# Kernel tuning notes

Hardware: AMD Instinct MI355X
Metric: run time of the kernel (lower is better)

The kernel has to match this reference:

```python
import jax, jax.numpy as jnp
import numpy as np

HID = 128
NLAYERS = 8
LAT = 32
DIM_IN = 63 + 15 + LAT  # pe(xyz,L=10)=3+60, pe(shift,L=2)=3+12, latent=32 -> 110


def _pe(x, L):
    # NeRF positional encoding, include_input=True, freq-major [sin3,cos3] per freq
    freqs = (2.0 ** jnp.arange(L)).astype(x.dtype)
    xf = x[..., None, :] * freqs[:, None]                      # [..., L, 3]
    sc = jnp.concatenate([jnp.sin(xf), jnp.cos(xf)], axis=-1)  # [..., L, 6]
    return jnp.concatenate([x, sc.reshape(*x.shape[:-1], 6 * L)], axis=-1)


def setup_inputs() -> dict:
    key = jax.random.key(0)
    ks = jax.random.split(key, 24)
    B, P, V = 2, 32768, 5023
    d = {}
    d["pts"] = jax.random.normal(ks[0], (B, P, 3), jnp.float32)
    d["deformed_mesh_pts"] = jax.random.normal(ks[1], (B, V, 3), jnp.float32)
    d["cano_verts"] = jax.random.normal(ks[2], (1, V, 3), jnp.float32)
    d["motion_latent"] = jax.random.normal(ks[3], (B, P, LAT), jnp.float32)
    for i in range(NLAYERS):
        fin = DIM_IN if i == 0 else (DIM_IN + HID if i == NLAYERS // 2 else HID)
        d[f"w{i}"] = jax.random.normal(ks[4 + i], (HID, fin), jnp.float32) / np.sqrt(fin).astype(np.float32)
        d[f"b{i}"] = jnp.zeros((HID,), jnp.float32)
    d["w_out"] = jax.random.normal(ks[20], (3, HID), jnp.float32) * 0.01
    d["b_out"] = jnp.zeros((3,), jnp.float32)
    return d


def reference(pts, deformed_mesh_pts, cano_verts, motion_latent,
              w0, b0, w1, b1, w2, b2, w3, b3, w4, b4, w5, b5, w6, b6, w7, b7,
              w_out, b_out):
    # mesh-guided shift per vertex
    mesh_shift = cano_verts - deformed_mesh_pts                 # [B,V,3]
    # point-to-point NN search (squared euclidean cdist + argmin)
    d2 = ((pts ** 2).sum(-1)[:, :, None]
          + (deformed_mesh_pts ** 2).sum(-1)[:, None, :]
          - 2.0 * jnp.einsum('bpc,bvc->bpv', pts, deformed_mesh_pts))  # [B,P,V]
    d2 = jnp.maximum(d2, 0.0)
    idx = jnp.argmin(d2, axis=-1)                               # [B,P]
    dist = jnp.min(d2, axis=-1)                                 # [B,P]
    weight = jnp.exp(-dist)[..., None]                          # 1/exp(dist)
    gidx = jnp.broadcast_to(idx[:, :, None], idx.shape + (3,))
    gshift = jnp.take_along_axis(mesh_shift, gidx, axis=1) * weight  # [B,P,3]
    # deformation MLP with skip connection at layer 4
    initial = jnp.concatenate([_pe(pts, 10), _pe(gshift, 2), motion_latent], axis=-1)
    ws = [w0, w1, w2, w3, w4, w5, w6, w7]
    bs = [b0, b1, b2, b3, b4, b5, b6, b7]
    x = initial
    last_feat = x
    for i in range(NLAYERS):
        inp = jnp.concatenate([initial, x], axis=-1) if i == NLAYERS // 2 else x
        x = inp @ ws[i].T + bs[i]
        last_feat = x  # pre-activation feature (out_feat_ls[-1])
        x = jax.nn.relu(x)
    mlp_shift = x @ w_out.T + b_out                             # [B,P,3]
    pts_shifts = gshift + mlp_shift
    return pts + pts_shifts, last_feat
```

## Files before the change

### kernel.cpp

```cpp
#include <hip/hip_runtime.h>
#include <math.h>

typedef unsigned short ushort_t;
typedef unsigned int   uint_t;
typedef __attribute__((ext_vector_type(8)))  short bf16x8;
typedef __attribute__((ext_vector_type(16))) float f32x16;
typedef __attribute__((ext_vector_type(2)))  float f32x2;

#define NPTS   65536
#define NV     5023
#define NVP    5120
#define NPRB   2560
#define LATD   32
#define KF     110
#define FSTR   112
#define MARGIN 2.0e-3f

__device__ __forceinline__ ushort_t f2bf(float f) {
  union { float f; unsigned u; } x; x.f = f;
  unsigned r = x.u + 0x7fffu + ((x.u >> 16) & 1u);
  return (ushort_t)(r >> 16);
}
__device__ __forceinline__ float bf2f(ushort_t u) {
  union { unsigned u; float f; } x; x.u = ((unsigned)u) << 16;
  return x.f;
}
__device__ __forceinline__ uint_t packsplit(float v) {
  const ushort_t h = f2bf(v);
  const ushort_t l = f2bf(v - bf2f(h));
  return (uint_t)h | ((uint_t)l << 16);
}

__device__ __forceinline__ void dbl_step(float& s, float& c) {
  const float t = s * c;
  const float cn = fmaf(-2.f * s, s, 1.f);
  s = t + t;
  c = cn;
}

__global__ __launch_bounds__(256) void k_prep(
    const float* __restrict__ dm,
    const float* __restrict__ w0, const float* __restrict__ w1,
    const float* __restrict__ w2, const float* __restrict__ w3,
    const float* __restrict__ w4, const float* __restrict__ w5,
    const float* __restrict__ w6, const float* __restrict__ w7,
    ushort_t* __restrict__ wsWh, ushort_t* __restrict__ wsWl,
    float4* __restrict__ vpreA, float4* __restrict__ vpreB)
{
  const int e = blockIdx.x * 256 + threadIdx.x;
  {
    const int p = e >> 14, local = e & 16383;
    const int j   = local & 7;
    const int lh  = (local >> 3) & 1;
    const int l31 = (local >> 4) & 31;
    const int tn  = (local >> 9) & 3;
    const int ks  = (local >> 11) & 7;
    const int n = tn*32 + l31;
    const int k = ks*16 + lh*8 + j;
    float v;
    if (p == 0)      v = (k < KF) ? w0[n*110 + k] : 0.f;
    else if (p == 1) v = w1[n*128 + k];
    else if (p == 2) v = w2[n*128 + k];
    else if (p == 3) v = w3[n*128 + k];
    else if (p == 4) v = (k < KF) ? w4[n*238 + k] : 0.f;
    else if (p == 5) v = w4[n*238 + KF + k];
    else if (p == 6) v = w5[n*128 + k];
    else if (p == 7) v = w6[n*128 + k];
    else             v = w7[n*128 + k];
    const ushort_t h = f2bf(v);
    wsWh[e] = h;
    wsWl[e] = f2bf(v - bf2f(h));
  }
  if (e < 2*NPRB) {
    const int b  = (e >= NPRB) ? 1 : 0;
    const int pr = e - b*NPRB;
    const float* __restrict__ dmb = dm + b*NV*3;
    const int v0 = 2*pr, v1 = v0 + 1;
    float x0=0.f, y0=0.f, z0=0.f, w0v=3.0e38f;
    float x1=0.f, y1=0.f, z1=0.f, w1v=3.0e38f;
    if (v0 < NV) {
      x0 = dmb[v0*3+0]; y0 = dmb[v0*3+1]; z0 = dmb[v0*3+2];
      w0v = fmaf(x0,x0, fmaf(y0,y0, z0*z0));
    }
    if (v1 < NV) {
      x1 = dmb[v1*3+0]; y1 = dmb[v1*3+1]; z1 = dmb[v1*3+2];
      w1v = fmaf(x1,x1, fmaf(y1,y1, z1*z1));
    }
    vpreA[b*NPRB + pr] = make_float4(x0, x1, y0, y1);
    vpreB[b*NPRB + pr] = make_float4(z0, z1, w0v, w1v);
  }
}

__global__ __launch_bounds__(256, 4) void k_nnfeat(
    const float* __restrict__ pts, const float* __restrict__ dm,
    const float* __restrict__ cano, const float* __restrict__ lat,
    const float4* __restrict__ vpreA, const float4* __restrict__ vpreB,
    uint_t* __restrict__ feat, float* __restrict__ base3)
{
  __shared__ __align__(16) float4 sVa[256];
  __shared__ __align__(16) float4 sVb[256];
  __shared__ float sD[64];
  __shared__ int   sI[64];

  const int tid = threadIdx.x;
  const int lane = tid & 63, w = tid >> 6;
  const int slot = lane >> 4, s = lane & 15;
  const int g0 = blockIdx.x * 64;
  const int b  = blockIdx.x >> 9;
  const int pbase = g0 + w*16 + slot*4;

  const float4* __restrict__ vA = vpreA + b*NPRB;
  const float4* __restrict__ vB = vpreB + b*NPRB;

  f32x2 MX[4], MY[4], MZ[4];
  float p2[4];
  #pragma unroll
  for (int j = 0; j < 4; ++j) {
    const float px = pts[(pbase+j)*3+0], py = pts[(pbase+j)*3+1], pz = pts[(pbase+j)*3+2];
    p2[j] = fmaf(px,px, fmaf(py,py, pz*pz));
    MX[j] = (f32x2){-2.f*px, -2.f*px};
    MY[j] = (f32x2){-2.f*py, -2.f*py};
    MZ[j] = (f32x2){-2.f*pz, -2.f*pz};
  }

  float gm[5][4];
  #pragma unroll
  for (int sc = 0; sc < 5; ++sc) {
    f32x2 m0 = {3.0e38f, 3.0e38f}, m1 = m0, m2 = m0, m3 = m0;
    #pragma unroll
    for (int h = 0; h < 2; ++h) {
      const int c = sc*2 + h;
      __syncthreads();
      sVa[tid] = vA[c*256 + tid];
      sVb[tid] = vB[c*256 + tid];
      __syncthreads();
      #pragma unroll 8
      for (int kk = 0; kk < 16; ++kk) {
        const int pr = kk*16 + s;
        const float4 qa = sVa[pr];
        const float4 qb = sVb[pr];
        const f32x2 xx = {qa.x, qa.y}, yy = {qa.z, qa.w};
        const f32x2 zz = {qb.x, qb.y}, ww = {qb.z, qb.w};
        f32x2 t;
        t = __builtin_elementwise_fma(xx, MX[0], ww);
        t = __builtin_elementwise_fma(yy, MY[0], t);
        t = __builtin_elementwise_fma(zz, MZ[0], t);
        m0 = __builtin_elementwise_min(m0, t);
        t = __builtin_elementwise_fma(xx, MX[1], ww);
        t = __builtin_elementwise_fma(yy, MY[1], t);
        t = __builtin_elementwise_fma(zz, MZ[1], t);
        m1 = __builtin_elementwise_min(m1, t);
        t = __builtin_elementwise_fma(xx, MX[2], ww);
        t = __builtin_elementwise_fma(yy, MY[2], t);
        t = __builtin_elementwise_fma(zz, MZ[2], t);
        m2 = __builtin_elementwise_min(m2, t);
        t = __builtin_elementwise_fma(xx, MX[3], ww);
        t = __builtin_elementwise_fma(yy, MY[3], t);
        t = __builtin_elementwise_fma(zz, MZ[3], t);
        m3 = __builtin_elementwise_min(m3, t);
      }
    }
    gm[sc][0] = fminf(m0.x, m0.y);
    gm[sc][1] = fminf(m1.x, m1.y);
    gm[sc][2] = fminf(m2.x, m2.y);
    gm[sc][3] = fminf(m3.x, m3.y);
  }

  float thr[4];
  #pragma unroll
  for (int j = 0; j < 4; ++j) {
    float mv = gm[0][j];
    #pragma unroll
    for (int sc = 1; sc < 5; ++sc) mv = fminf(mv, gm[sc][j]);
    #pragma unroll
    for (int off = 1; off <= 8; off <<= 1)
      mv = fminf(mv, __shfl_xor(mv, off, 64));
    thr[j] = mv + MARGIN;
  }

  float bs[4]; int bi[4];
  #pragma unroll
  for (int j = 0; j < 4; ++j) { bs[j] = 3.4e38f; bi[j] = 0; }
  uint_t hm = 0;
  #pragma unroll
  for (int sc = 0; sc < 5; ++sc)
    if (gm[sc][0] <= thr[0] || gm[sc][1] <= thr[1] ||
        gm[sc][2] <= thr[2] || gm[sc][3] <= thr[3]) hm |= (1u << sc);
  while (hm) {
    const int sc = __ffs(hm) - 1; hm &= hm - 1;
    const int prb = sc*512;
    #pragma unroll 4
    for (int kk = 0; kk < 32; ++kk) {
      const int pr = prb + kk*16 + s;
      const float4 qa = vA[pr];
      const float4 qb = vB[pr];
      const int vi0 = 2*pr;
      #pragma unroll
      for (int j = 0; j < 4; ++j) {
        const float px = -0.5f*MX[j].x, py = -0.5f*MY[j].x, pz = -0.5f*MZ[j].x;
        {
          const float dot = fmaf(px, qa.x, fmaf(py, qa.z, pz*qb.x));
          float d2 = fmaf(-2.f, dot, p2[j] + qb.z);
          d2 = fmaxf(d2, 0.f);
          if (d2 < bs[j]) { bs[j] = d2; bi[j] = vi0; }
        }
        {
          const float dot = fmaf(px, qa.y, fmaf(py, qa.w, pz*qb.y));
          float d2 = fmaf(-2.f, dot, p2[j] + qb.w);
          d2 = fmaxf(d2, 0.f);
          if (d2 < bs[j]) { bs[j] = d2; bi[j] = vi0 + 1; }
        }
      }
    }
  }

  #pragma unroll
  for (int off = 1; off <= 8; off <<= 1) {
    #pragma unroll
    for (int j = 0; j < 4; ++j) {
      const float ob = __shfl_xor(bs[j], off, 64);
      const int   oi = __shfl_xor(bi[j], off, 64);
      const bool take = (ob < bs[j]) || ((ob == bs[j]) && (oi < bi[j]));
      if (take) { bs[j] = ob; bi[j] = oi; }
    }
  }
  if (s == 0) {
    #pragma unroll
    for (int j = 0; j < 4; ++j) {
      sD[w*16 + slot*4 + j] = bs[j];
      sI[w*16 + slot*4 + j] = bi[j];
    }
  }
  __syncthreads();

  const int p = tid & 63, slice = tid >> 6;
  const int g = g0 + p;
  const float wd = sD[p];
  const int   wi = sI[p];
  const float* __restrict__ dmb = dm + b * NV * 3;

  const float qx = pts[g*3+0], qy = pts[g*3+1], qz = pts[g*3+2];
  const float wgt = expf(-wd);
  const float sx = (cano[wi*3+0] - dmb[wi*3+0]) * wgt;
  const float sy = (cano[wi*3+1] - dmb[wi*3+1]) * wgt;
  const float sz = (cano[wi*3+2] - dmb[wi*3+2]) * wgt;

  uint_t* __restrict__ fr = feat + (size_t)g * FSTR;

  if (slice == 0) {
    base3[g*3+0] = qx + sx; base3[g*3+1] = qy + sy; base3[g*3+2] = qz + sz;
    fr[0] = packsplit(qx); fr[1] = packsplit(qy); fr[2] = packsplit(qz);
    float s0,c0,s1,c1,s2,c2;
    sincosf(qx,&s0,&c0); sincosf(qy,&s1,&c1); sincosf(qz,&s2,&c2);
    #pragma unroll
    for (int f = 0; f < 3; ++f) {
      const int k = 3 + 6*f;
      fr[k+0]=packsplit(s0); fr[k+1]=packsplit(s1); fr[k+2]=packsplit(s2);
      fr[k+3]=packsplit(c0); fr[k+4]=packsplit(c1); fr[k+5]=packsplit(c2);
      if (f < 2) { dbl_step(s0,c0); dbl_step(s1,c1); dbl_step(s2,c2); }
    }
    fr[110] = 0; fr[111] = 0;
  } else if (slice == 1) {
    float s0,c0,s1,c1,s2,c2;
    sincosf(qx*8.f,&s0,&c0); sincosf(qy*8.f,&s1,&c1); sincosf(qz*8.f,&s2,&c2);
    #pragma unroll
    for (int f = 3; f < 7; ++f) {
      const int k = 3 + 6*f;
      fr[k+0]=packsplit(s0); fr[k+1]=packsplit(s1); fr[k+2]=packsplit(s2);
      fr[k+3]=packsplit(c0); fr[k+4]=packsplit(c1); fr[k+5]=packsplit(c2);
      if (f < 6) { dbl_step(s0,c0); dbl_step(s1,c1); dbl_step(s2,c2); }
    }
  } else if (slice == 2) {
    float s0,c0,s1,c1,s2,c2;
    sincosf(qx*128.f,&s0,&c0); sincosf(qy*128.f,&s1,&c1); sincosf(qz*128.f,&s2,&c2);
    #pragma unroll
    for (int f = 7; f < 10; ++f) {
      const int k = 3 + 6*f;
      fr[k+0]=packsplit(s0); fr[k+1]=packsplit(s1); fr[k+2]=packsplit(s2);
      fr[k+3]=packsplit(c0); fr[k+4]=packsplit(c1); fr[k+5]=packsplit(c2);
      if (f < 9) { dbl_step(s0,c0); dbl_step(s1,c1); dbl_step(s2,c2); }
    }
    #pragma unroll
    for (int j = 0; j < 16; ++j) fr[78+j] = packsplit(lat[g*LATD + j]);
  } else {
    fr[63]=packsplit(sx); fr[64]=packsplit(sy); fr[65]=packsplit(sz);
    float s0,c0,s1,c1,s2,c2;
    sincosf(sx,&s0,&c0); sincosf(sy,&s1,&c1); sincosf(sz,&s2,&c2);
    #pragma unroll
    for (int f = 0; f < 2; ++f) {
      const int k = 66 + 6*f;
      fr[k+0]=packsplit(s0); fr[k+1]=packsplit(s1); fr[k+2]=packsplit(s2);
      fr[k+3]=packsplit(c0); fr[k+4]=packsplit(c1); fr[k+5]=packsplit(c2);
      if (f < 1) { dbl_step(s0,c0); dbl_step(s1,c1); dbl_step(s2,c2); }
    }
    #pragma unroll
    for (int j = 16; j < 32; ++j) fr[78+j] = packsplit(lat[g*LATD + j]);
  }
}


union U4 { uint_t u[4]; bf16x8 v; };

__device__ __forceinline__ void zero4(f32x16 (&a)[4]) {
  #pragma unroll
  for (int i = 0; i < 4; ++i) a[i] = (f32x16)(0.f);
}

__device__ __forceinline__ void load_feat_frags(
    const uint_t* __restrict__ fr, bf16x8 (&Xh)[8], bf16x8 (&Xl)[8], int lh)
{
  #pragma unroll
  for (int ks = 0; ks < 7; ++ks) {
    const int k0 = ks*16 + lh*8;
    const uint4 ua = *(const uint4*)(fr + k0);
    const uint4 ub = *(const uint4*)(fr + k0 + 4);
    U4 H, L;
    H.u[0] = (ua.x & 0xffffu) | (ua.y << 16);
    H.u[1] = (ua.z & 0xffffu) | (ua.w << 16);
    H.u[2] = (ub.x & 0xffffu) | (ub.y << 16);
    H.u[3] = (ub.z & 0xffffu) | (ub.w << 16);
    L.u[0] = (ua.x >> 16) | (ua.y & 0xffff0000u);
    L.u[1] = (ua.z >> 16) | (ua.w & 0xffff0000u);
    L.u[2] = (ub.x >> 16) | (ub.y & 0xffff0000u);
    L.u[3] = (ub.z >> 16) | (ub.w & 0xffff0000u);
    Xh[ks] = H.v; Xl[ks] = L.v;
  }
}

__device__ __forceinline__ void load_slab(bf16x8 (&wh)[4], bf16x8 (&wl)[4],
    const ushort_t* __restrict__ Wh, const ushort_t* __restrict__ Wl,
    int ks, int l31, int lh)
{
  const int lo = l31*16 + lh*8;
  #pragma unroll
  for (int tn = 0; tn < 4; ++tn) {
    const int off = (ks*4 + tn)*512 + lo;
    wh[tn] = *(const bf16x8*)(Wh + off);
    wl[tn] = *(const bf16x8*)(Wl + off);
  }
}

__device__ __forceinline__ void mfma_slab(f32x16 (&acc)[4],
    const bf16x8 (&wh)[4], const bf16x8 (&wl)[4],
    const bf16x8& xh, const bf16x8& xl)
{
  #pragma unroll
  for (int tn = 0; tn < 4; ++tn) {
    acc[tn] = __builtin_amdgcn_mfma_f32_32x32x16_bf16(wh[tn], xh, acc[tn], 0,0,0);
    acc[tn] = __builtin_amdgcn_mfma_f32_32x32x16_bf16(wl[tn], xh, acc[tn], 0,0,0);
    acc[tn] = __builtin_amdgcn_mfma_f32_32x32x16_bf16(wh[tn], xl, acc[tn], 0,0,0);
  }
}

template<int NKS, bool TAIL>
__device__ __forceinline__ void run_panel(f32x16 (&acc)[4],
    const ushort_t* __restrict__ Wh, const ushort_t* __restrict__ Wl,
    const ushort_t* __restrict__ WhN, const ushort_t* __restrict__ WlN,
    bf16x8 (&wbh)[2][4], bf16x8 (&wbl)[2][4],
    const bf16x8 (&Xh)[8], const bf16x8 (&Xl)[8], int l31, int lh)
{
  #pragma unroll
  for (int ks = 0; ks < NKS; ++ks) {
    const int b = ks & 1;
    mfma_slab(acc, wbh[b], wbl[b], Xh[ks], Xl[ks]);
    if (ks + 2 < NKS) {
      load_slab(wbh[b], wbl[b], Wh, Wl, ks + 2, l31, lh);
    } else if (TAIL) {
      load_slab(wbh[b], wbl[b], WhN, WlN, ks & 1, l31, lh);
    }
  }
}

__device__ __forceinline__ void bias_relu(f32x16 (&acc)[4],
    const float* __restrict__ bias, int lh)
{
  #pragma unroll
  for (int tn = 0; tn < 4; ++tn)
    #pragma unroll
    for (int b = 0; b < 4; ++b) {
      const float4 b4 = *(const float4*)(bias + tn*32 + 8*b + 4*lh);
      acc[tn][4*b+0] = fmaxf(acc[tn][4*b+0] + b4.x, 0.f);
      acc[tn][4*b+1] = fmaxf(acc[tn][4*b+1] + b4.y, 0.f);
      acc[tn][4*b+2] = fmaxf(acc[tn][4*b+2] + b4.z, 0.f);
      acc[tn][4*b+3] = fmaxf(acc[tn][4*b+3] + b4.w, 0.f);
    }
}

__device__ __forceinline__ void build_frags(const f32x16 (&acc)[4],
    bf16x8 (&Xh)[8], bf16x8 (&Xl)[8], int lh)
{
  #pragma unroll
  for (int ks = 0; ks < 8; ++ks) {
    const int tn = ks >> 1;
    const int rb = 8*(ks & 1);
    const float f0 = acc[tn][rb+0], f1 = acc[tn][rb+1];
    const float f2 = acc[tn][rb+2], f3 = acc[tn][rb+3];
    const float f4 = acc[tn][rb+4], f5 = acc[tn][rb+5];
    const float f6 = acc[tn][rb+6], f7 = acc[tn][rb+7];
    const ushort_t h0=f2bf(f0), h1=f2bf(f1), h2=f2bf(f2), h3=f2bf(f3);
    const ushort_t h4=f2bf(f4), h5=f2bf(f5), h6=f2bf(f6), h7=f2bf(f7);
    const uint_t hA0 = (uint_t)h0 | ((uint_t)h1 << 16);
    const uint_t hA1 = (uint_t)h2 | ((uint_t)h3 << 16);
    const uint_t hB0 = (uint_t)h4 | ((uint_t)h5 << 16);
    const uint_t hB1 = (uint_t)h6 | ((uint_t)h7 << 16);
    const uint_t lA0 = (uint_t)f2bf(f0 - bf2f(h0)) | ((uint_t)f2bf(f1 - bf2f(h1)) << 16);
    const uint_t lA1 = (uint_t)f2bf(f2 - bf2f(h2)) | ((uint_t)f2bf(f3 - bf2f(h3)) << 16);
    const uint_t lB0 = (uint_t)f2bf(f4 - bf2f(h4)) | ((uint_t)f2bf(f5 - bf2f(h5)) << 16);
    const uint_t lB1 = (uint_t)f2bf(f6 - bf2f(h6)) | ((uint_t)f2bf(f7 - bf2f(h7)) << 16);
    const uint_t sh0 = lh ? hA0 : hB0, sh1 = lh ? hA1 : hB1;
    const uint_t sl0 = lh ? lA0 : lB0, sl1 = lh ? lA1 : lB1;
    const uint_t rh0 = __shfl_xor(sh0, 32, 64), rh1 = __shfl_xor(sh1, 32, 64);
    const uint_t rl0 = __shfl_xor(sl0, 32, 64), rl1 = __shfl_xor(sl1, 32, 64);
    U4 H, L;
    H.u[0] = lh ? rh0 : hA0;  H.u[1] = lh ? rh1 : hA1;
    H.u[2] = lh ? hB0 : rh0;  H.u[3] = lh ? hB1 : rh1;
    L.u[0] = lh ? rl0 : lA0;  L.u[1] = lh ? rl1 : lA1;
    L.u[2] = lh ? lB0 : rl0;  L.u[3] = lh ? lB1 : rl1;
    Xh[ks] = H.v; Xl[ks] = L.v;
  }
}

__global__ __launch_bounds__(256, 2) void k_mlp(
    const uint_t* __restrict__ feat, const float* __restrict__ base3,
    const ushort_t* __restrict__ wsWh, const ushort_t* __restrict__ wsWl,
    const float* __restrict__ b0, const float* __restrict__ b1,
    const float* __restrict__ b2, const float* __restrict__ b3,
    const float* __restrict__ b4, const float* __restrict__ b5,
    const float* __restrict__ b6, const float* __restrict__ b7,
    const float* __restrict__ w_out, const float* __restrict__ b_out,
    float* __restrict__ out)
{
  __shared__ __align__(16) float sF[4][32*132];
  __shared__ __align__(16) float sB[8*128 + 384 + 4];

  const int tid  = threadIdx.x;
  const int lane = tid & 63, wid = tid >> 6;
  const int l31 = lane & 31, lh = lane >> 5;
  const int p0 = blockIdx.x * 128 + wid * 32;

  {
    const float* bsp[8] = {b0,b1,b2,b3,b4,b5,b6,b7};
    if (tid < 128) {
      #pragma unroll
      for (int l = 0; l < 8; ++l) sB[l*128 + tid] = bsp[l][tid];
    }
    for (int i = tid; i < 384; i += 256) sB[1024 + i] = w_out[i];
    if (tid < 3) sB[1408 + tid] = b_out[tid];
  }

  const uint_t* __restrict__ fr = feat + (size_t)(p0 + l31) * FSTR;

  bf16x8 Xh[8], Xl[8];
  bf16x8 wbh[2][4], wbl[2][4];
  f32x16 acc[4];

  load_slab(wbh[0], wbl[0], wsWh, wsWl, 0, l31, lh);
  load_slab(wbh[1], wbl[1], wsWh, wsWl, 1, l31, lh);
  load_feat_frags(fr, Xh, Xl, lh);
  __syncthreads();

  zero4(acc);
  run_panel<7,true>(acc, wsWh + 0*16384, wsWl + 0*16384,
                         wsWh + 1*16384, wsWl + 1*16384, wbh, wbl, Xh, Xl, l31, lh);
  bias_relu(acc, sB + 0*128, lh);
  build_frags(acc, Xh, Xl, lh);

  zero4(acc);
  run_panel<8,true>(acc, wsWh + 1*16384, wsWl + 1*16384,
                         wsWh + 2*16384, wsWl + 2*16384, wbh, wbl, Xh, Xl, l31, lh);
  bias_relu(acc, sB + 1*128, lh);
  build_frags(acc, Xh, Xl, lh);

  zero4(acc);
  run_panel<8,true>(acc, wsWh + 2*16384, wsWl + 2*16384,
                         wsWh + 3*16384, wsWl + 3*16384, wbh, wbl, Xh, Xl, l31, lh);
  bias_relu(acc, sB + 2*128, lh);
  build_frags(acc, Xh, Xl, lh);

  zero4(acc);
  run_panel<8,true>(acc, wsWh + 3*16384, wsWl + 3*16384,
                         wsWh + 5*16384, wsWl + 5*16384, wbh, wbl, Xh, Xl, l31, lh);
  bias_relu(acc, sB + 3*128, lh);
  build_frags(acc, Xh, Xl, lh);

  zero4(acc);
  run_panel<8,true>(acc, wsWh + 5*16384, wsWl + 5*16384,
                         wsWh + 4*16384, wsWl + 4*16384, wbh, wbl, Xh, Xl, l31, lh);
  load_feat_frags(fr, Xh, Xl, lh);
  run_panel<7,true>(acc, wsWh + 4*16384, wsWl + 4*16384,
                         wsWh + 6*16384, wsWl + 6*16384, wbh, wbl, Xh, Xl, l31, lh);
  bias_relu(acc, sB + 4*128, lh);
  build_frags(acc, Xh, Xl, lh);

  zero4(acc);
  run_panel<8,true>(acc, wsWh + 6*16384, wsWl + 6*16384,
                         wsWh + 7*16384, wsWl + 7*16384, wbh, wbl, Xh, Xl, l31, lh);
  bias_relu(acc, sB + 5*128, lh);
  build_frags(acc, Xh, Xl, lh);

  zero4(acc);
  run_panel<8,true>(acc, wsWh + 7*16384, wsWl + 7*16384,
                         wsWh + 8*16384, wsWl + 8*16384, wbh, wbl, Xh, Xl, l31, lh);
  bias_relu(acc, sB + 6*128, lh);
  build_frags(acc, Xh, Xl, lh);

  zero4(acc);
  run_panel<8,false>(acc, wsWh + 8*16384, wsWl + 8*16384,
                          (const ushort_t*)0, (const ushort_t*)0, wbh, wbl, Xh, Xl, l31, lh);

  float* __restrict__ sFw = &sF[wid][0];
  #pragma unroll
  for (int tn = 0; tn < 4; ++tn)
    #pragma unroll
    for (int b = 0; b < 4; ++b) {
      const int n0 = tn*32 + 8*b + 4*lh;
      const float4 bv = *(const float4*)(sB + 7*128 + n0);
      const float v0 = acc[tn][4*b+0] + bv.x;
      const float v1 = acc[tn][4*b+1] + bv.y;
      const float v2 = acc[tn][4*b+2] + bv.z;
      const float v3 = acc[tn][4*b+3] + bv.w;
      *(float4*)(sFw + l31*132 + n0) = make_float4(v0, v1, v2, v3);
      acc[tn][4*b+0] = fmaxf(v0, 0.f);
      acc[tn][4*b+1] = fmaxf(v1, 0.f);
      acc[tn][4*b+2] = fmaxf(v2, 0.f);
      acc[tn][4*b+3] = fmaxf(v3, 0.f);
    }

  asm volatile("s_waitcnt lgkmcnt(0)" ::: "memory");
  __builtin_amdgcn_sched_barrier(0);

  float* __restrict__ out1 = out + (size_t)NPTS * 3;
  #pragma unroll
  for (int i = 0; i < 16; ++i) {
    const int idx = i*64 + lane;
    const int p = idx >> 5, q = idx & 31;
    const float4 v = *(const float4*)(sFw + p*132 + q*4);
    *(float4*)(out1 + (size_t)(p0 + p)*128 + q*4) = v;
  }

  float dotc[3];
  #pragma unroll
  for (int c = 0; c < 3; ++c) {
    float a = 0.f;
    #pragma unroll
    for (int tn = 0; tn < 4; ++tn)
      #pragma unroll
      for (int b = 0; b < 4; ++b) {
        const int n0 = tn*32 + 8*b + 4*lh;
        const float4 w4 = *(const float4*)(sB + 1024 + c*128 + n0);
        a = fmaf(acc[tn][4*b+0], w4.x, a);
        a = fmaf(acc[tn][4*b+1], w4.y, a);
        a = fmaf(acc[tn][4*b+2], w4.z, a);
        a = fmaf(acc[tn][4*b+3], w4.w, a);
      }
    a += __shfl_xor(a, 32, 64);
    dotc[c] = a;
  }
  if (lh == 0) {
    const int g = p0 + l31;
    #pragma unroll
    for (int c = 0; c < 3; ++c)
      out[g*3 + c] = base3[g*3 + c] + dotc[c] + sB[1408 + c];
  }
}

extern "C" void kernel_launch(void* const* d_in, const int* in_sizes, int n_in,
                              void* d_out, int out_size, void* d_ws, size_t ws_size,
                              hipStream_t stream)
{
  const float* pts  = (const float*)d_in[0];
  const float* dm   = (const float*)d_in[1];
  const float* cano = (const float*)d_in[2];
  const float* lat  = (const float*)d_in[3];
  const float* w[8]; const float* b[8];
  for (int i = 0; i < 8; ++i) {
    w[i] = (const float*)d_in[4 + 2*i];
    b[i] = (const float*)d_in[5 + 2*i];
  }
  const float* w_out = (const float*)d_in[20];
  const float* b_out = (const float*)d_in[21];
  float* out = (float*)d_out;

  uint_t*   feat  = (uint_t*)d_ws;
  float*    base3 = (float*)((char*)d_ws + (size_t)NPTS*FSTR*4);
  ushort_t* wsWh  = (ushort_t*)((char*)base3 + (size_t)NPTS*3*4);
  ushort_t* wsWl  = wsWh + 147456;
  float4*   vpreA = (float4*)(wsWl + 147456);
  float4*   vpreB = vpreA + 2*NPRB;

  k_prep<<<576, 256, 0, stream>>>(dm,
      w[0],w[1],w[2],w[3],w[4],w[5],w[6],w[7], wsWh, wsWl, vpreA, vpreB);
  k_nnfeat<<<1024, 256, 0, stream>>>(pts, dm, cano, lat, vpreA, vpreB, feat, base3);
  k_mlp<<<NPTS/128, 256, 0, stream>>>(feat, base3, wsWh, wsWl,
      b[0],b[1],b[2],b[3],b[4],b[5],b[6],b[7], w_out, b_out, out);
}
```

Before: 258.4 us.

## Process 8 points per thread in NN search with double-buffered vertex tiles

```diff
diff --git a/kernel.cpp b/kernel.cpp
--- a/kernel.cpp
+++ b/kernel.cpp
@@ -91,31 +91,31 @@
   }
 }
 
-__global__ __launch_bounds__(256, 4) void k_nnfeat(
+__global__ __launch_bounds__(256, 2) void k_nnfeat(
     const float* __restrict__ pts, const float* __restrict__ dm,
     const float* __restrict__ cano, const float* __restrict__ lat,
     const float4* __restrict__ vpreA, const float4* __restrict__ vpreB,
     uint_t* __restrict__ feat, float* __restrict__ base3)
 {
-  __shared__ __align__(16) float4 sVa[256];
-  __shared__ __align__(16) float4 sVb[256];
-  __shared__ float sD[64];
-  __shared__ int   sI[64];
+  __shared__ __align__(16) float4 sVa[2][256];
+  __shared__ __align__(16) float4 sVb[2][256];
+  __shared__ float sD[128];
+  __shared__ int   sI[128];
 
   const int tid = threadIdx.x;
   const int lane = tid & 63, w = tid >> 6;
   const int slot = lane >> 4, s = lane & 15;
-  const int g0 = blockIdx.x * 64;
-  const int b  = blockIdx.x >> 9;
-  const int pbase = g0 + w*16 + slot*4;
+  const int g0 = blockIdx.x * 128;
+  const int b  = blockIdx.x >> 8;
+  const int pbase = g0 + w*32 + slot*8;
 
   const float4* __restrict__ vA = vpreA + b*NPRB;
   const float4* __restrict__ vB = vpreB + b*NPRB;
 
-  f32x2 MX[4], MY[4], MZ[4];
-  float p2[4];
-  #pragma unroll
-  for (int j = 0; j < 4; ++j) {
+  f32x2 MX[8], MY[8], MZ[8];
+  float p2[8];
+  #pragma unroll
+  for (int j = 0; j < 8; ++j) {
     const float px = pts[(pbase+j)*3+0], py = pts[(pbase+j)*3+1], pz = pts[(pbase+j)*3+2];
     p2[j] = fmaf(px,px, fmaf(py,py, pz*pz));
     MX[j] = (f32x2){-2.f*px, -2.f*px};
@@ -123,52 +123,56 @@
     MZ[j] = (f32x2){-2.f*pz, -2.f*pz};
   }
 
-  float gm[5][4];
-  #pragma unroll
-  for (int sc = 0; sc < 5; ++sc) {
-    f32x2 m0 = {3.0e38f, 3.0e38f}, m1 = m0, m2 = m0, m3 = m0;
-    #pragma unroll
-    for (int h = 0; h < 2; ++h) {
-      const int c = sc*2 + h;
+  sVa[0][tid] = vA[tid];
+  sVb[0][tid] = vB[tid];
+  __syncthreads();
+
+  float gm[5][8];
+  f32x2 m[8];
+  int cur = 0;
+  #pragma unroll
+  for (int c = 0; c < 10; ++c) {
+    if ((c & 1) == 0) {
+      #pragma unroll
+      for (int j = 0; j < 8; ++j) m[j] = (f32x2){3.0e38f, 3.0e38f};
+    }
+    float4 ra, rb;
+    if (c + 1 < 10) {
+      ra = vA[(c+1)*256 + tid];
+      rb = vB[(c+1)*256 + tid];
+    }
+    #pragma unroll 4
+    for (int kk = 0; kk < 16; ++kk) {
+      const int pr = kk*16 + s;
+      const float4 qa = sVa[cur][pr];
+      const float4 qb = sVb[cur][pr];
+      const f32x2 xx = {qa.x, qa.y}, yy = {qa.z, qa.w};
+      const f32x2 zz = {qb.x, qb.y}, ww = {qb.z, qb.w};
+      #pragma unroll
+      for (int j = 0; j < 8; ++j) {
+        f32x2 t;
+        t = __builtin_elementwise_fma(xx, MX[j], ww);
+        t = __builtin_elementwise_fma(yy, MY[j], t);
+        t = __builtin_elementwise_fma(zz, MZ[j], t);
+        m[j] = __builtin_elementwise_min(m[j], t);
+      }
+    }
+    if (c + 1 < 10) {
       __syncthreads();
-      sVa[tid] = vA[c*256 + tid];
-      sVb[tid] = vB[c*256 + tid];
+      sVa[cur^1][tid] = ra;
+      sVb[cur^1][tid] = rb;
       __syncthreads();
-      #pragma unroll 8
-      for (int kk = 0; kk < 16; ++kk) {
-        const int pr = kk*16 + s;
-        const float4 qa = sVa[pr];
-        const float4 qb = sVb[pr];
-        const f32x2 xx = {qa.x, qa.y}, yy = {qa.z, qa.w};
-        const f32x2 zz = {qb.x, qb.y}, ww = {qb.z, qb.w};
-        f32x2 t;
-        t = __builtin_elementwise_fma(xx, MX[0], ww);
-        t = __builtin_elementwise_fma(yy, MY[0], t);
-        t = __builtin_elementwise_fma(zz, MZ[0], t);
-        m0 = __builtin_elementwise_min(m0, t);
-        t = __builtin_elementwise_fma(xx, MX[1], ww);
-        t = __builtin_elementwise_fma(yy, MY[1], t);
-        t = __builtin_elementwise_fma(zz, MZ[1], t);
-        m1 = __builtin_elementwise_min(m1, t);
-        t = __builtin_elementwise_fma(xx, MX[2], ww);
-        t = __builtin_elementwise_fma(yy, MY[2], t);
-        t = __builtin_elementwise_fma(zz, MZ[2], t);
-        m2 = __builtin_elementwise_min(m2, t);
-        t = __builtin_elementwise_fma(xx, MX[3], ww);
-        t = __builtin_elementwise_fma(yy, MY[3], t);
-        t = __builtin_elementwise_fma(zz, MZ[3], t);
-        m3 = __builtin_elementwise_min(m3, t);
-      }
-    }
-    gm[sc][0] = fminf(m0.x, m0.y);
-    gm[sc][1] = fminf(m1.x, m1.y);
-    gm[sc][2] = fminf(m2.x, m2.y);
-    gm[sc][3] = fminf(m3.x, m3.y);
-  }
-
-  float thr[4];
-  #pragma unroll
-  for (int j = 0; j < 4; ++j) {
+      cur ^= 1;
+    }
+    if (c & 1) {
+      #pragma unroll
+      for (int j = 0; j < 8; ++j) gm[c>>1][j] = fminf(m[j].x, m[j].y);
+    }
+  }
+
+  float thr[8];
+  #pragma unroll
+  for (int j = 0; j < 8; ++j) {
     float mv = gm[0][j];
     #pragma unroll
     for (int sc = 1; sc < 5; ++sc) mv = fminf(mv, gm[sc][j]);
@@ -178,14 +182,17 @@
     thr[j] = mv + MARGIN;
   }
 
-  float bs[4]; int bi[4];
-  #pragma unroll
-  for (int j = 0; j < 4; ++j) { bs[j] = 3.4e38f; bi[j] = 0; }
+  float bs[8]; int bi[8];
+  #pragma unroll
+  for (int j = 0; j < 8; ++j) { bs[j] = 3.4e38f; bi[j] = 0; }
   uint_t hm = 0;
   #pragma unroll
-  for (int sc = 0; sc < 5; ++sc)
-    if (gm[sc][0] <= thr[0] || gm[sc][1] <= thr[1] ||
-        gm[sc][2] <= thr[2] || gm[sc][3] <= thr[3]) hm |= (1u << sc);
+  for (int sc = 0; sc < 5; ++sc) {
+    bool hit = false;
+    #pragma unroll
+    for (int j = 0; j < 8; ++j) hit = hit || (gm[sc][j] <= thr[j]);
+    if (hit) hm |= (1u << sc);
+  }
   while (hm) {
     const int sc = __ffs(hm) - 1; hm &= hm - 1;
     const int prb = sc*512;
@@ -196,7 +203,7 @@
       const float4 qb = vB[pr];
       const int vi0 = 2*pr;
       #pragma unroll
-      for (int j = 0; j < 4; ++j) {
+      for (int j = 0; j < 8; ++j) {
         const float px = -0.5f*MX[j].x, py = -0.5f*MY[j].x, pz = -0.5f*MZ[j].x;
         {
           const float dot = fmaf(px, qa.x, fmaf(py, qa.z, pz*qb.x));
@@ -217,7 +224,7 @@
   #pragma unroll
   for (int off = 1; off <= 8; off <<= 1) {
     #pragma unroll
-    for (int j = 0; j < 4; ++j) {
+    for (int j = 0; j < 8; ++j) {
       const float ob = __shfl_xor(bs[j], off, 64);
       const int   oi = __shfl_xor(bi[j], off, 64);
       const bool take = (ob < bs[j]) || ((ob == bs[j]) && (oi < bi[j]));
@@ -226,14 +233,14 @@
   }
   if (s == 0) {
     #pragma unroll
-    for (int j = 0; j < 4; ++j) {
-      sD[w*16 + slot*4 + j] = bs[j];
-      sI[w*16 + slot*4 + j] = bi[j];
+    for (int j = 0; j < 8; ++j) {
+      sD[w*32 + slot*8 + j] = bs[j];
+      sI[w*32 + slot*8 + j] = bi[j];
     }
   }
   __syncthreads();
 
-  const int p = tid & 63, slice = tid >> 6;
+  const int p = tid & 127, slice = tid >> 7;
   const int g = g0 + p;
   const float wd = sD[p];
   const int   wi = sI[p];
@@ -259,9 +266,6 @@
       fr[k+3]=packsplit(c0); fr[k+4]=packsplit(c1); fr[k+5]=packsplit(c2);
       if (f < 2) { dbl_step(s0,c0); dbl_step(s1,c1); dbl_step(s2,c2); }
     }
-    fr[110] = 0; fr[111] = 0;
-  } else if (slice == 1) {
-    float s0,c0,s1,c1,s2,c2;
     sincosf(qx*8.f,&s0,&c0); sincosf(qy*8.f,&s1,&c1); sincosf(qz*8.f,&s2,&c2);
     #pragma unroll
     for (int f = 3; f < 7; ++f) {
@@ -270,7 +274,7 @@
       fr[k+3]=packsplit(c0); fr[k+4]=packsplit(c1); fr[k+5]=packsplit(c2);
       if (f < 6) { dbl_step(s0,c0); dbl_step(s1,c1); dbl_step(s2,c2); }
     }
-  } else if (slice == 2) {
+  } else {
     float s0,c0,s1,c1,s2,c2;
     sincosf(qx*128.f,&s0,&c0); sincosf(qy*128.f,&s1,&c1); sincosf(qz*128.f,&s2,&c2);
     #pragma unroll
@@ -280,11 +284,7 @@
       fr[k+3]=packsplit(c0); fr[k+4]=packsplit(c1); fr[k+5]=packsplit(c2);
       if (f < 9) { dbl_step(s0,c0); dbl_step(s1,c1); dbl_step(s2,c2); }
     }
-    #pragma unroll
-    for (int j = 0; j < 16; ++j) fr[78+j] = packsplit(lat[g*LATD + j]);
-  } else {
     fr[63]=packsplit(sx); fr[64]=packsplit(sy); fr[65]=packsplit(sz);
-    float s0,c0,s1,c1,s2,c2;
     sincosf(sx,&s0,&c0); sincosf(sy,&s1,&c1); sincosf(sz,&s2,&c2);
     #pragma unroll
     for (int f = 0; f < 2; ++f) {
@@ -294,7 +294,8 @@
       if (f < 1) { dbl_step(s0,c0); dbl_step(s1,c1); dbl_step(s2,c2); }
     }
     #pragma unroll
-    for (int j = 16; j < 32; ++j) fr[78+j] = packsplit(lat[g*LATD + j]);
+    for (int j = 0; j < 32; ++j) fr[78+j] = packsplit(lat[g*LATD + j]);
+    fr[110] = 0; fr[111] = 0;
   }
 }
 
@@ -590,7 +591,7 @@
 
   k_prep<<<576, 256, 0, stream>>>(dm,
       w[0],w[1],w[2],w[3],w[4],w[5],w[6],w[7], wsWh, wsWl, vpreA, vpreB);
-  k_nnfeat<<<1024, 256, 0, stream>>>(pts, dm, cano, lat, vpreA, vpreB, feat, base3);
+  k_nnfeat<<<512, 256, 0, stream>>>(pts, dm, cano, lat, vpreA, vpreB, feat, base3);
   k_mlp<<<NPTS/128, 256, 0, stream>>>(feat, base3, wsWh, wsWl,
       b[0],b[1],b[2],b[3],b[4],b[5],b[6],b[7], w_out, b_out, out);
 }
```

New measurement: 327.9 us. +26.9%, slower.
